# Optimization experiments

Measured on AMD Instinct MI355X. Metric: run time of the kernel, lower is better.

The kernel has to match this reference:

```python
import jax, jax.numpy as jnp
import numpy as np

NUM_ATOMS = 50000
NUM_EDGES = 200000  # even: edges come in (fwd, rev) pairs
D_V, D_E, D_H = 133, 14, 256
DEPTH = 3


def setup_inputs() -> dict:
    key = jax.random.key(0)
    ks = jax.random.split(key, 12)
    half = NUM_EDGES // 2
    src = jax.random.randint(ks[0], (half,), 0, NUM_ATOMS)
    dst = jax.random.randint(ks[1], (half,), 0, NUM_ATOMS)
    v = jnp.concatenate([src, dst])
    w = jnp.concatenate([dst, src])
    edge_index = jnp.stack([v, w])  # [2, E]
    rev_edge_index = jnp.concatenate([jnp.arange(half) + half, jnp.arange(half)])

    def lin(k, out_d, in_d):
        return jax.random.normal(k, (out_d, in_d), jnp.float32) / np.sqrt(in_d)

    return {
        "V": jax.random.normal(ks[2], (NUM_ATOMS, D_V), jnp.float32),
        "E_feat": jax.random.normal(ks[3], (NUM_EDGES, D_E), jnp.float32),
        "edge_index": edge_index,
        "rev_edge_index": rev_edge_index,
        "Wi_atom": lin(ks[4], D_H, D_V),
        "Wi_bond": lin(ks[5], D_H, D_V + D_E),
        "Wh_atom": lin(ks[6], D_H, D_H),
        "Wh_bond": lin(ks[7], D_H, D_H),
        "Wf_atom": lin(ks[8], D_H, D_H),
        "Wf_bond": lin(ks[9], D_H, D_H),
        "Wo_atom": lin(ks[10], D_H, D_V + D_H),
    }


def _sum_and_max_into_atoms(H_e, w_idx, num_atoms):
    a_sum = jax.ops.segment_sum(H_e, w_idx, num_segments=num_atoms)
    a_max = jax.ops.segment_max(H_e, w_idx, num_segments=num_atoms)
    a_max = jnp.where(jnp.isfinite(a_max), a_max, 0.0)  # empty segments -> 0
    return a_sum, a_max


def _fuse(H, m, Wf):
    # Fusion(kind='mlp', residual=True), dropout=0:
    # residual update with a small MLP on the combined signal
    return H + jax.nn.relu((H + m) @ Wf.T)


def reference(V, E_feat, edge_index, rev_edge_index, Wi_atom, Wi_bond,
              Wh_atom, Wh_bond, Wf_atom, Wf_bond, Wo_atom):
    tau = jax.nn.relu
    num_atoms = V.shape[0]
    v = edge_index[0]
    w = edge_index[1]

    H_a = tau(V @ Wi_atom.T)                                        # [N, d_h]
    H_b = tau(jnp.concatenate([V[v], E_feat], axis=1) @ Wi_bond.T)  # [E, d_h]

    for _ in range(1, DEPTH):
        a_sum, a_max = _sum_and_max_into_atoms(H_b, w, num_atoms)
        gate = a_sum * a_max
        m_a = gate @ Wh_atom.T
        H_a = _fuse(H_a, m_a, Wf_atom)

        M_b = a_sum[v] - H_b[rev_edge_index]
        m_b = M_b @ Wh_bond.T
        H_b = _fuse(H_b, m_b, Wf_bond)

    a_sum, _ = _sum_and_max_into_atoms(H_b, w, num_atoms)
    H_atom = tau(jnp.concatenate([V, a_sum], axis=1) @ Wo_atom.T)   # [N, d_h]
    return H_atom
```

## Files before the change

### kernel.cpp

```cpp
#include <hip/hip_runtime.h>
#include <hip/hip_bf16.h>

#define NATOM 50000
#define NEDGE 200000
#define HALF  100000
#define DV    133
#define DE    14
#define DH    256
#define KVP   160
#define NBLK_SCAN ((NATOM + 255) / 256)

typedef __bf16  bf16x8 __attribute__((ext_vector_type(8)));
typedef __bf16  bf16x4 __attribute__((ext_vector_type(4)));
typedef float   f32x4  __attribute__((ext_vector_type(4)));

__device__ __forceinline__ void gll16(const void* g, void* l) {
    __builtin_amdgcn_global_load_lds(
        (const __attribute__((address_space(1))) unsigned int*)g,
        (__attribute__((address_space(3))) unsigned int*)l, 16, 0, 0);
}
__device__ __forceinline__ void drain_barrier() {
    __builtin_amdgcn_s_waitcnt(0);
    __syncthreads();
}
__device__ __forceinline__ int swz(int row, int byteInRow) {
    return row * 512 + (byteInRow ^ ((row & 7) << 4));
}


struct DArgs {
    const float* Vf; const float* Ef; const float* asumf;
    const int* vidx;
    const __bf16* W1; const __bf16* W2;
    __bf16* C; float* Cf;
    int M;
};

template<int MODE, int KITERS>
__global__ __launch_bounds__(512, 4) void dgemm(DArgs g) {
    const int tid = threadIdx.x;
    const int lane = tid & 63, wv = tid >> 6;
    const int quad = lane >> 4, l16 = lane & 15;
    const int wr = (wv >> 2) * 64, wc = (wv & 3) * 64;
    const int gr0 = blockIdx.x * 128;

    int vrow[4]; const float* epp[4];
#pragma unroll
    for (int m = 0; m < 4; ++m) {
        int r = gr0 + wr + m * 16 + l16;
        if (r > g.M - 1) r = g.M - 1;
        vrow[m] = (MODE == 1) ? g.vidx[r] : r;
        epp[m] = (MODE == 1) ? (g.Ef + (size_t)r * DE) : nullptr;
    }

    f32x4 acc[16];
#pragma unroll
    for (int i = 0; i < 16; ++i) acc[i] = (f32x4){0.f, 0.f, 0.f, 0.f};

#pragma unroll
    for (int kk = 0; kk < KITERS; ++kk) {
        bf16x8 af[4];
#pragma unroll
        for (int m = 0; m < 4; ++m) {
            const int cb = kk * 32 + quad * 8;
            if (MODE != 2 || kk < 5) {
                const float* vp = g.Vf + (size_t)vrow[m] * DV;
                if (kk < 4) {
                    f32x4 x0, x1;
                    __builtin_memcpy(&x0, vp + cb, 16);
                    __builtin_memcpy(&x1, vp + cb + 4, 16);
#pragma unroll
                    for (int j = 0; j < 4; ++j) {
                        af[m][j] = (__bf16)x0[j]; af[m][4 + j] = (__bf16)x1[j];
                    }
                } else {
#pragma unroll
                    for (int j = 0; j < 8; ++j) {
                        int c = cb + j; float y = 0.f;
                        if (c < DV) y = vp[c];
                        else if (MODE == 1 && c < DV + DE) y = epp[m][c - DV];
                        af[m][j] = (__bf16)y;
                    }
                }
            } else {
                const float* sp = g.asumf + (size_t)vrow[m] * DH + (kk - 5) * 32 + quad * 8;
                f32x4 s0 = *(const f32x4*)sp, s1 = *(const f32x4*)(sp + 4);
#pragma unroll
                for (int j = 0; j < 4; ++j) {
                    af[m][j] = (__bf16)s0[j]; af[m][4 + j] = (__bf16)s1[j];
                }
            }
        }
        bf16x8 bfv[4];
#pragma unroll
        for (int n = 0; n < 4; ++n) {
            int col = wc + n * 16 + l16;
            const __bf16* wp;
            if (MODE == 2 && kk >= 5) wp = g.W2 + (size_t)col * DH  + (kk - 5) * 32 + quad * 8;
            else                      wp = g.W1 + (size_t)col * KVP + kk * 32 + quad * 8;
            bfv[n] = *(const bf16x8*)wp;
        }
#pragma unroll
        for (int m = 0; m < 4; ++m)
#pragma unroll
            for (int n = 0; n < 4; ++n)
                acc[m * 4 + n] = __builtin_amdgcn_mfma_f32_16x16x32_bf16(
                    af[m], bfv[n], acc[m * 4 + n], 0, 0, 0);
    }

#pragma unroll
    for (int m = 0; m < 4; ++m)
#pragma unroll
    for (int n = 0; n < 4; ++n)
#pragma unroll
    for (int r = 0; r < 4; ++r) {
        int gr = gr0 + wr + m * 16 + quad * 4 + r;
        if (gr < g.M) {
            int col = wc + n * 16 + l16;
            float v = acc[m * 4 + n][r];
            v = v > 0.f ? v : 0.f;
            if (MODE == 2) g.Cf[(size_t)gr * DH + col] = v;
            else           g.C [(size_t)gr * DH + col] = (__bf16)v;
        }
    }
}

struct FArgs {
    const float* asumf; const __bf16* asumb; const __bf16* amaxb;
    const int* vidx;
    const __bf16* W1; const __bf16* W2;
    __bf16* H;
    int M;
};

template<int BOND>
__global__ __launch_bounds__(512, 2) void fgemm(FArgs g) {
    __shared__ __bf16 Hlds[32768];
    __shared__ __bf16 Alds[32768];
    const int tid = threadIdx.x;
    const int lane = tid & 63, wv = tid >> 6;
    const int quad = lane >> 4, l16 = lane & 15;
    const int wr = (wv >> 2) * 64;
    const int wc = (wv & 3) * 64;
    const int bid = blockIdx.x;

    int garow[4];
    if (!BOND) {
#pragma unroll
        for (int fr = 0; fr < 4; ++fr) {
            int r = bid * 128 + wr + fr * 16 + l16;
            if (r > g.M - 1) r = g.M - 1;
            garow[fr] = r;
        }
    }

#pragma unroll
    for (int it = 0; it < 8; ++it) {
        int unit = it * 512 + wv * 64 + lane;
        int lr = unit >> 5, u16 = unit & 31;
        int swzoff = (u16 * 16) ^ ((lr & 7) << 4);
        int srow;
        if (BOND) { int sl = bid * 64 + (lr & 63); if (sl > g.M - 1) sl = g.M - 1;
                    srow = (lr < 64) ? sl : HALF + sl; }
        else      { srow = bid * 128 + lr; if (srow > g.M - 1) srow = g.M - 1; }
        gll16((const char*)g.H + (size_t)srow * 512 + swzoff,
              (char*)Hlds + it * 8192 + wv * 1024);
        if (BOND) {
            int sl = bid * 64 + (lr & 63); if (sl > g.M - 1) sl = g.M - 1;
            int gA = (lr < 64) ? sl : HALF + sl;
            int grow = g.vidx[gA];
            gll16((const char*)g.asumb + (size_t)grow * 512 + swzoff,
                  (char*)Alds + it * 8192 + wv * 1024);
        }
    }
    drain_barrier();

    f32x4 acc[16];
#pragma unroll
    for (int i = 0; i < 16; ++i) acc[i] = (f32x4){0.f, 0.f, 0.f, 0.f};

#pragma unroll
    for (int kk = 0; kk < 8; ++kk) {
        const int cb = kk * 32 + quad * 8;
        bf16x8 mf[4];
#pragma unroll
        for (int fr = 0; fr < 4; ++fr) {
            int lr = wr + fr * 16 + l16;
            if (BOND) {
                bf16x8 a = *(const bf16x8*)((const char*)Alds + swz(lr, cb * 2));
                bf16x8 h = *(const bf16x8*)((const char*)Hlds + swz(lr ^ 64, cb * 2));
#pragma unroll
                for (int j = 0; j < 8; ++j)
                    mf[fr][j] = (__bf16)((float)a[j] - (float)h[j]);
            } else {
                const float* s = g.asumf + (size_t)garow[fr] * DH + cb;
                f32x4 s0 = *(const f32x4*)s, s1 = *(const f32x4*)(s + 4);
                bf16x8 mx = *(const bf16x8*)(g.amaxb + (size_t)garow[fr] * DH + cb);
#pragma unroll
                for (int j = 0; j < 4; ++j) {
                    mf[fr][j]     = (__bf16)(s0[j] * (float)mx[j]);
                    mf[fr][4 + j] = (__bf16)(s1[j] * (float)mx[4 + j]);
                }
            }
        }
        bf16x8 wf[4];
#pragma unroll
        for (int fc = 0; fc < 4; ++fc)
            wf[fc] = *(const bf16x8*)(g.W1 + (size_t)(wc + fc * 16 + l16) * DH + cb);
#pragma unroll
        for (int fc = 0; fc < 4; ++fc)
#pragma unroll
            for (int fr = 0; fr < 4; ++fr)
                acc[fc * 4 + fr] = __builtin_amdgcn_mfma_f32_16x16x32_bf16(
                    wf[fc], mf[fr], acc[fc * 4 + fr], 0, 0, 0);
    }
    drain_barrier();

#pragma unroll
    for (int fc = 0; fc < 4; ++fc)
#pragma unroll
    for (int fr = 0; fr < 4; ++fr) {
        int row = wr + fr * 16 + l16;
        int colb = wc + fc * 16 + quad * 4;
        int off = swz(row, colb * 2);
        bf16x4 h = *(const bf16x4*)((const char*)Hlds + off);
        bf16x4 t;
#pragma unroll
        for (int j = 0; j < 4; ++j)
            t[j] = (__bf16)((float)h[j] + acc[fc * 4 + fr][j]);
        *(bf16x4*)((char*)Alds + off) = t;
    }
    drain_barrier();

#pragma unroll
    for (int i = 0; i < 16; ++i) acc[i] = (f32x4){0.f, 0.f, 0.f, 0.f};
#pragma unroll
    for (int kk = 0; kk < 8; ++kk) {
        const int cb = kk * 32 + quad * 8;
        bf16x8 tf[4];
#pragma unroll
        for (int fr = 0; fr < 4; ++fr) {
            int lr = wr + fr * 16 + l16;
            tf[fr] = *(const bf16x8*)((const char*)Alds + swz(lr, cb * 2));
        }
        bf16x8 wf[4];
#pragma unroll
        for (int fc = 0; fc < 4; ++fc)
            wf[fc] = *(const bf16x8*)(g.W2 + (size_t)(wc + fc * 16 + l16) * DH + cb);
#pragma unroll
        for (int fc = 0; fc < 4; ++fc)
#pragma unroll
            for (int fr = 0; fr < 4; ++fr)
                acc[fc * 4 + fr] = __builtin_amdgcn_mfma_f32_16x16x32_bf16(
                    wf[fc], tf[fr], acc[fc * 4 + fr], 0, 0, 0);
    }

#pragma unroll
    for (int fc = 0; fc < 4; ++fc)
#pragma unroll
    for (int fr = 0; fr < 4; ++fr) {
        int row = wr + fr * 16 + l16;
        int colb = wc + fc * 16 + quad * 4;
        int off = swz(row, colb * 2);
        bf16x4 h = *(const bf16x4*)((const char*)Hlds + off);
        bf16x4 o;
#pragma unroll
        for (int j = 0; j < 4; ++j) {
            float v = acc[fc * 4 + fr][j];
            v = v > 0.f ? v : 0.f;
            o[j] = (__bf16)((float)h[j] + v);
        }
        *(bf16x4*)((char*)Hlds + off) = o;
    }
    drain_barrier();

#pragma unroll
    for (int it = 0; it < 8; ++it) {
        int unit = it * 512 + tid;
        int lr = unit >> 5, u16 = unit & 31;
        bool ok; int srow;
        if (BOND) { int sl = bid * 64 + (lr & 63); ok = sl < g.M;
                    srow = (lr < 64) ? sl : HALF + sl; }
        else      { srow = bid * 128 + lr; ok = srow < g.M; }
        if (ok) {
            bf16x8 v = *(const bf16x8*)((const char*)Hlds + swz(lr, u16 * 16));
            *(bf16x8*)((char*)g.H + (size_t)srow * 512 + u16 * 16) = v;
        }
    }
}

__global__ void count_deg(const int* __restrict__ widx, int* __restrict__ cnt) {
    int e = blockIdx.x * 256 + threadIdx.x;
    if (e < NEDGE) atomicAdd(&cnt[widx[e]], 1);
}

__global__ __launch_bounds__(256) void scan_p1(const int* __restrict__ cnt,
                                               int* __restrict__ rowptr,
                                               int* __restrict__ bsum) {
    __shared__ int sm[256];
    const int tid = threadIdx.x;
    const int i = blockIdx.x * 256 + tid;
    int v = (i < NATOM) ? cnt[i] : 0;
    sm[tid] = v;
    __syncthreads();
    for (int off = 1; off < 256; off <<= 1) {
        int t = (tid >= off) ? sm[tid - off] : 0;
        __syncthreads();
        sm[tid] += t;
        __syncthreads();
    }
    if (i < NATOM) rowptr[i] = sm[tid] - v;
    if (tid == 255) bsum[blockIdx.x] = sm[255];
}

__global__ __launch_bounds__(256) void scan_p2(int* __restrict__ bsum) {
    __shared__ int sm[256];
    const int tid = threadIdx.x;
    int v = (tid < NBLK_SCAN) ? bsum[tid] : 0;
    sm[tid] = v;
    __syncthreads();
    for (int off = 1; off < 256; off <<= 1) {
        int t = (tid >= off) ? sm[tid - off] : 0;
        __syncthreads();
        sm[tid] += t;
        __syncthreads();
    }
    if (tid < NBLK_SCAN) bsum[tid] = sm[tid] - v;
    if (tid == 255) bsum[NBLK_SCAN] = sm[255];
}

__global__ __launch_bounds__(256) void scan_p3(int* __restrict__ rowptr,
                                               int* __restrict__ cursor,
                                               const int* __restrict__ bsum) {
    const int i = blockIdx.x * 256 + threadIdx.x;
    if (i < NATOM) {
        int r = rowptr[i] + bsum[blockIdx.x];
        rowptr[i] = r;
        cursor[i] = r;
    }
    if (i == 0) rowptr[NATOM] = bsum[NBLK_SCAN];
}

__global__ void fill_csr(const int* __restrict__ widx, int* __restrict__ cursor,
                         int* __restrict__ eid) {
    int e = blockIdx.x * 256 + threadIdx.x;
    if (e >= NEDGE) return;
    int pos = atomicAdd(&cursor[widx[e]], 1);
    eid[pos] = e;
}

template<int WITHMAX>
__global__ __launch_bounds__(256) void seg_reduce(
    const __bf16* __restrict__ Hb, const int* __restrict__ rowptr,
    const int* __restrict__ eid,
    float* __restrict__ asum, __bf16* __restrict__ asumb,
    __bf16* __restrict__ amaxb)
{
    int a = blockIdx.x * 4 + (threadIdx.x >> 6);
    if (a >= NATOM) return;
    const int lane = threadIdx.x & 63;
    const int beg = rowptr[a], end = rowptr[a + 1];
    float s0 = 0.f, s1 = 0.f, s2 = 0.f, s3 = 0.f;
    float m0 = 0.f, m1 = 0.f, m2 = 0.f, m3 = 0.f;
    for (int i = beg; i < end; ++i) {
        int e = eid[i];
        bf16x4 h = *(const bf16x4*)(Hb + (size_t)e * DH + lane * 4);
        float v0 = (float)h[0], v1 = (float)h[1], v2 = (float)h[2], v3 = (float)h[3];
        s0 += v0; s1 += v1; s2 += v2; s3 += v3;
        if (WITHMAX) {
            m0 = fmaxf(m0, v0); m1 = fmaxf(m1, v1);
            m2 = fmaxf(m2, v2); m3 = fmaxf(m3, v3);
        }
    }
    size_t o = (size_t)a * DH + lane * 4;
    *(f32x4*)(asum + o) = (f32x4){s0, s1, s2, s3};
    if (WITHMAX) {
        bf16x4 sv; sv[0] = (__bf16)s0; sv[1] = (__bf16)s1; sv[2] = (__bf16)s2; sv[3] = (__bf16)s3;
        *(bf16x4*)(asumb + o) = sv;
        bf16x4 mv; mv[0] = (__bf16)m0; mv[1] = (__bf16)m1; mv[2] = (__bf16)m2; mv[3] = (__bf16)m3;
        *(bf16x4*)(amaxb + o) = mv;
    }
}

__global__ void pad_w2(const float* __restrict__ src, __bf16* __restrict__ dst,
                       int srcld, int coloff, int KS, int KD) {
    int i = blockIdx.x * 256 + threadIdx.x;
    if (i >= 256 * KD) return;
    int n = i / KD, c = i - n * KD;
    dst[i] = (c < KS) ? (__bf16)src[(size_t)n * srcld + coloff + c] : (__bf16)0.f;
}

static inline int cdiv(long a, long b) { return (int)((a + b - 1) / b); }

extern "C" void kernel_launch(void* const* d_in, const int* in_sizes, int n_in,
                              void* d_out, int out_size, void* d_ws, size_t ws_size,
                              hipStream_t stream) {
    const float* V    = (const float*)d_in[0];
    const float* Ef   = (const float*)d_in[1];
    const int*   ei   = (const int*)d_in[2];
    const int*   rev  = (const int*)d_in[3];
    const float* Wi_a = (const float*)d_in[4];
    const float* Wi_b = (const float*)d_in[5];
    const float* Wh_a = (const float*)d_in[6];
    const float* Wh_b = (const float*)d_in[7];
    const float* Wf_a = (const float*)d_in[8];
    const float* Wf_b = (const float*)d_in[9];
    const float* Wo   = (const float*)d_in[10];
    float* out = (float*)d_out;
    (void)rev;

    const int* vidx = ei;
    const int* widx = ei + NEDGE;

    char* ws = (char*)d_ws;
    __bf16* Hb    = (__bf16*)(ws + 0);
    __bf16* Ha    = (__bf16*)(ws + 102400000);
    float*  asum  = (float*) (ws + 128000000);
    __bf16* asumb = (__bf16*)(ws + 179200000);
    __bf16* amaxb = (__bf16*)(ws + 204800000);
    __bf16* Wia   = (__bf16*)(ws + 230400000);
    __bf16* Wib   = (__bf16*)(ws + 230481920);
    __bf16* Wo1   = (__bf16*)(ws + 230563840);
    __bf16* Wo2   = (__bf16*)(ws + 230645760);
    __bf16* Wha   = (__bf16*)(ws + 230776832);
    __bf16* Whb   = (__bf16*)(ws + 230907904);
    __bf16* Wfa   = (__bf16*)(ws + 231038976);
    __bf16* Wfb   = (__bf16*)(ws + 231170048);
    int*  rowptr  = (int*)(ws + 231301120);
    int*  cursor  = (int*)(ws + 231501312);
    int*  eid     = (int*)(ws + 231701504);
    int*  bsum    = (int*)(ws + 232501504);
    (void)ws_size;

    hipMemsetAsync(cursor, 0, NATOM * sizeof(int), stream);
    count_deg<<<cdiv(NEDGE, 256), 256, 0, stream>>>(widx, cursor);
    scan_p1<<<NBLK_SCAN, 256, 0, stream>>>(cursor, rowptr, bsum);
    scan_p2<<<1, 256, 0, stream>>>(bsum);
    scan_p3<<<NBLK_SCAN, 256, 0, stream>>>(rowptr, cursor, bsum);
    fill_csr<<<cdiv(NEDGE, 256), 256, 0, stream>>>(widx, cursor, eid);

    pad_w2<<<cdiv(256 * KVP, 256), 256, 0, stream>>>(Wi_a, Wia, DV, 0, DV, KVP);
    pad_w2<<<cdiv(256 * KVP, 256), 256, 0, stream>>>(Wi_b, Wib, DV + DE, 0, DV + DE, KVP);
    pad_w2<<<cdiv(256 * KVP, 256), 256, 0, stream>>>(Wo, Wo1, DV + DH, 0, DV, KVP);
    pad_w2<<<cdiv(256 * DH, 256), 256, 0, stream>>>(Wo, Wo2, DV + DH, DV, DH, DH);
    pad_w2<<<cdiv(256 * DH, 256), 256, 0, stream>>>(Wh_a, Wha, DH, 0, DH, DH);
    pad_w2<<<cdiv(256 * DH, 256), 256, 0, stream>>>(Wh_b, Whb, DH, 0, DH, DH);
    pad_w2<<<cdiv(256 * DH, 256), 256, 0, stream>>>(Wf_a, Wfa, DH, 0, DH, DH);
    pad_w2<<<cdiv(256 * DH, 256), 256, 0, stream>>>(Wf_b, Wfb, DH, 0, DH, DH);

    {
        DArgs d{}; d.Vf = V; d.W1 = Wia; d.C = Ha; d.M = NATOM;
        dgemm<0, 5><<<cdiv(NATOM, 128), 512, 0, stream>>>(d);
    }
    {
        DArgs d{}; d.Vf = V; d.Ef = Ef; d.vidx = vidx; d.W1 = Wib; d.C = Hb; d.M = NEDGE;
        dgemm<1, 5><<<cdiv(NEDGE, 128), 512, 0, stream>>>(d);
    }

    for (int it = 0; it < 2; ++it) {
        seg_reduce<1><<<cdiv(NATOM, 4), 256, 0, stream>>>(Hb, rowptr, eid, asum, asumb, amaxb);
        {
            FArgs f{}; f.asumf = asum; f.amaxb = amaxb;
            f.W1 = Wha; f.W2 = Wfa; f.H = Ha; f.M = NATOM;
            fgemm<0><<<cdiv(NATOM, 128), 512, 0, stream>>>(f);
        }
        {
            FArgs f{}; f.asumb = asumb; f.vidx = vidx;
            f.W1 = Whb; f.W2 = Wfb; f.H = Hb; f.M = HALF;
            fgemm<1><<<cdiv(HALF, 64), 512, 0, stream>>>(f);
        }
    }

    seg_reduce<0><<<cdiv(NATOM, 4), 256, 0, stream>>>(Hb, rowptr, eid, asum, nullptr, nullptr);
    {
        DArgs d{}; d.Vf = V; d.asumf = asum; d.W1 = Wo1; d.W2 = Wo2; d.Cf = out; d.M = NATOM;
        dgemm<2, 13><<<cdiv(NATOM, 128), 512, 0, stream>>>(d);
    }
}
```

Before: 1.003 ms.

## Drop H tile from LDS in fused GEMM, read H from global to raise occupancy

The fused two-GEMM kernel no longer stages the H tile in shared memory. H values for the reverse-edge subtraction and both residual adds are read straight from global memory, so only one 64 KB LDS buffer remains. Launch bounds go from 2 to 4 blocks per CU to use the freed LDS. This trades LDS capacity for more scattered global reads of H, which may be served by cache, and it adds a barrier before the buffer is reused.

Result: slower. 1.282 ms (+27.8%).

```diff
diff --git a/kernel.cpp b/kernel.cpp
--- a/kernel.cpp
+++ b/kernel.cpp
@@ -134,9 +134,8 @@
 };
 
 template<int BOND>
-__global__ __launch_bounds__(512, 2) void fgemm(FArgs g) {
-    __shared__ __bf16 Hlds[32768];
-    __shared__ __bf16 Alds[32768];
+__global__ __launch_bounds__(512, 4) void fgemm(FArgs g) {
+    __shared__ __bf16 Tlds[32768];
     const int tid = threadIdx.x;
     const int lane = tid & 63, wv = tid >> 6;
     const int quad = lane >> 4, l16 = lane & 15;
@@ -154,26 +153,20 @@
         }
     }
 
-#pragma unroll
-    for (int it = 0; it < 8; ++it) {
-        int unit = it * 512 + wv * 64 + lane;
-        int lr = unit >> 5, u16 = unit & 31;
-        int swzoff = (u16 * 16) ^ ((lr & 7) << 4);
-        int srow;
-        if (BOND) { int sl = bid * 64 + (lr & 63); if (sl > g.M - 1) sl = g.M - 1;
-                    srow = (lr < 64) ? sl : HALF + sl; }
-        else      { srow = bid * 128 + lr; if (srow > g.M - 1) srow = g.M - 1; }
-        gll16((const char*)g.H + (size_t)srow * 512 + swzoff,
-              (char*)Hlds + it * 8192 + wv * 1024);
-        if (BOND) {
+    if (BOND) {
+#pragma unroll
+        for (int it = 0; it < 8; ++it) {
+            int unit = it * 512 + wv * 64 + lane;
+            int lr = unit >> 5, u16 = unit & 31;
+            int swzoff = (u16 * 16) ^ ((lr & 7) << 4);
             int sl = bid * 64 + (lr & 63); if (sl > g.M - 1) sl = g.M - 1;
             int gA = (lr < 64) ? sl : HALF + sl;
             int grow = g.vidx[gA];
             gll16((const char*)g.asumb + (size_t)grow * 512 + swzoff,
-                  (char*)Alds + it * 8192 + wv * 1024);
-        }
-    }
-    drain_barrier();
+                  (char*)Tlds + it * 8192 + wv * 1024);
+        }
+        drain_barrier();
+    }
 
     f32x4 acc[16];
 #pragma unroll
@@ -187,8 +180,10 @@
         for (int fr = 0; fr < 4; ++fr) {
             int lr = wr + fr * 16 + l16;
             if (BOND) {
-                bf16x8 a = *(const bf16x8*)((const char*)Alds + swz(lr, cb * 2));
-                bf16x8 h = *(const bf16x8*)((const char*)Hlds + swz(lr ^ 64, cb * 2));
+                bf16x8 a = *(const bf16x8*)((const char*)Tlds + swz(lr, cb * 2));
+                int sl = bid * 64 + (lr & 63); if (sl > g.M - 1) sl = g.M - 1;
+                int hrow = (lr < 64) ? HALF + sl : sl;
+                bf16x8 h = *(const bf16x8*)(g.H + (size_t)hrow * DH + cb);
 #pragma unroll
                 for (int j = 0; j < 8; ++j)
                     mf[fr][j] = (__bf16)((float)a[j] - (float)h[j]);
@@ -214,7 +209,7 @@
                 acc[fc * 4 + fr] = __builtin_amdgcn_mfma_f32_16x16x32_bf16(
                     wf[fc], mf[fr], acc[fc * 4 + fr], 0, 0, 0);
     }
-    drain_barrier();
+    if (BOND) drain_barrier();
 
 #pragma unroll
     for (int fc = 0; fc < 4; ++fc)
@@ -222,13 +217,16 @@
     for (int fr = 0; fr < 4; ++fr) {
         int row = wr + fr * 16 + l16;
         int colb = wc + fc * 16 + quad * 4;
-        int off = swz(row, colb * 2);
-        bf16x4 h = *(const bf16x4*)((const char*)Hlds + off);
+        int gOut;
+        if (BOND) { int sl = bid * 64 + (row & 63); if (sl > g.M - 1) sl = g.M - 1;
+                    gOut = (row < 64) ? sl : HALF + sl; }
+        else      { gOut = bid * 128 + row; if (gOut > g.M - 1) gOut = g.M - 1; }
+        bf16x4 h = *(const bf16x4*)(g.H + (size_t)gOut * DH + colb);
         bf16x4 t;
 #pragma unroll
         for (int j = 0; j < 4; ++j)
             t[j] = (__bf16)((float)h[j] + acc[fc * 4 + fr][j]);
-        *(bf16x4*)((char*)Alds + off) = t;
+        *(bf16x4*)((char*)Tlds + swz(row, colb * 2)) = t;
     }
     drain_barrier();
 
@@ -241,7 +239,7 @@
 #pragma unroll
         for (int fr = 0; fr < 4; ++fr) {
             int lr = wr + fr * 16 + l16;
-            tf[fr] = *(const bf16x8*)((const char*)Alds + swz(lr, cb * 2));
+            tf[fr] = *(const bf16x8*)((const char*)Tlds + swz(lr, cb * 2));
         }
         bf16x8 wf[4];
 #pragma unroll
@@ -254,6 +252,7 @@
                 acc[fc * 4 + fr] = __builtin_amdgcn_mfma_f32_16x16x32_bf16(
                     wf[fc], tf[fr], acc[fc * 4 + fr], 0, 0, 0);
     }
+    drain_barrier();
 
 #pragma unroll
     for (int fc = 0; fc < 4; ++fc)
@@ -261,8 +260,11 @@
     for (int fr = 0; fr < 4; ++fr) {
         int row = wr + fr * 16 + l16;
         int colb = wc + fc * 16 + quad * 4;
-        int off = swz(row, colb * 2);
-        bf16x4 h = *(const bf16x4*)((const char*)Hlds + off);
+        int gOut;
+        if (BOND) { int sl = bid * 64 + (row & 63); if (sl > g.M - 1) sl = g.M - 1;
+                    gOut = (row < 64) ? sl : HALF + sl; }
+        else      { gOut = bid * 128 + row; if (gOut > g.M - 1) gOut = g.M - 1; }
+        bf16x4 h = *(const bf16x4*)(g.H + (size_t)gOut * DH + colb);
         bf16x4 o;
 #pragma unroll
         for (int j = 0; j < 4; ++j) {
@@ -270,7 +272,7 @@
             v = v > 0.f ? v : 0.f;
             o[j] = (__bf16)((float)h[j] + v);
         }
-        *(bf16x4*)((char*)Hlds + off) = o;
+        *(bf16x4*)((char*)Tlds + swz(row, colb * 2)) = o;
     }
     drain_barrier();
 
@@ -283,7 +285,7 @@
                     srow = (lr < 64) ? sl : HALF + sl; }
         else      { srow = bid * 128 + lr; ok = srow < g.M; }
         if (ok) {
-            bf16x8 v = *(const bf16x8*)((const char*)Hlds + swz(lr, u16 * 16));
+            bf16x8 v = *(const bf16x8*)((const char*)Tlds + swz(lr, u16 * 16));
             *(bf16x8*)((char*)g.H + (size_t)srow * 512 + u16 * 16) = v;
         }
     }
```
